# Kernel tuning notes

Measured on AMD Instinct MI355X. Metric: run time of the kernel, lower is better.

The kernel has to match this reference:

```python
import math
import itertools
import jax, jax.numpy as jnp
import numpy as np

SEQ_LEN = 16
D_IN = 2048
TSS = 3          # temporal_set_size
D_OUT = 1128
PE_SCALE = 0.1
N_SUPPORT = 5
N_QUERIES = 1
LN_EPS = 1e-5


def _pos_enc(seq_len, d_model):
    pos = np.arange(seq_len, dtype=np.float32)[:, None]
    div = np.exp(np.arange(0, d_model, 2, dtype=np.float32) * -(math.log(10000.0) / d_model))
    pe = np.zeros((seq_len, d_model), dtype=np.float32)
    pe[:, 0::2] = np.sin(pos * div) * PE_SCALE
    pe[:, 1::2] = np.cos(pos * div) * PE_SCALE
    return jnp.asarray(pe)


def _tuples(seq_len, k):
    return np.asarray(list(itertools.combinations(range(seq_len), k)), dtype=np.int32)  # [T, k]


def setup_inputs() -> dict:
    key = jax.random.key(0)
    ks = jax.random.split(key, 8)
    return {
        "support_set": jax.random.normal(ks[0], (N_SUPPORT, SEQ_LEN, D_IN), jnp.float32),
        "queries": jax.random.normal(ks[1], (N_QUERIES, SEQ_LEN, D_IN), jnp.float32),
        "support_labels": jnp.arange(N_SUPPORT, dtype=jnp.int64),
        "wk": jax.random.normal(ks[2], (D_OUT, D_IN * TSS), jnp.float32) * 0.02,
        "bk": jax.random.normal(ks[3], (D_OUT,), jnp.float32) * 0.02,
        "wv": jax.random.normal(ks[4], (D_OUT, D_IN * TSS), jnp.float32) * 0.02,
        "bv": jax.random.normal(ks[5], (D_OUT,), jnp.float32) * 0.02,
        "gamma": jnp.ones((D_OUT,), jnp.float32),
        "beta": jnp.zeros((D_OUT,), jnp.float32),
    }


def _layer_norm(x, gamma, beta):
    mu = jnp.mean(x, axis=-1, keepdims=True)
    var = jnp.mean(jnp.square(x - mu), axis=-1, keepdims=True)
    return (x - mu) * jax.lax.rsqrt(var + LN_EPS) * gamma + beta


def reference(support_set, queries, support_labels, wk, bk, wv, bv, gamma, beta):
    tup = _tuples(SEQ_LEN, TSS)                      # [T, 3] static
    T = tup.shape[0]                                 # tuples_len = C(16,3) = 560
    pe = _pos_enc(SEQ_LEN, D_IN)                     # [S, D_IN]

    s = support_set + pe                             # [5, S, D_IN]
    q = queries + pe                                 # [1, S, D_IN]

    # gather frame tuples and flatten: [n, T, 3*D_IN]
    s_t = s[:, tup, :].reshape(N_SUPPORT, T, TSS * D_IN)
    q_t = q[:, tup, :].reshape(N_QUERIES, T, TSS * D_IN)

    s_ks = _layer_norm(s_t @ wk.T + bk, gamma, beta)  # [5, T, D_OUT]
    q_ks = _layer_norm(q_t @ wk.T + bk, gamma, beta)  # [1, T, D_OUT]
    s_vs = s_t @ wv.T + bv                            # [5, T, D_OUT]
    q_vs = q_t @ wv.T + bv                            # [1, T, D_OUT]

    # _extract_class_indices returns the label value itself -> direct row gather
    ck = s_ks[support_labels]                         # [C, T, D_OUT]
    cv = s_vs[support_labels]                         # [C, T, D_OUT]

    scores = jnp.einsum('qtd,csd->cqts', q_ks, ck) / math.sqrt(D_OUT)  # [C, Q, T, T]
    attn = jax.nn.softmax(scores, axis=-1)            # softmax over support tuples
    proto = jnp.einsum('cqts,csd->cqtd', attn, cv)    # [C, Q, T, D_OUT]

    diff = q_vs[None] - proto                         # [C, Q, T, D_OUT]
    dist = -jnp.sum(diff * diff, axis=(-2, -1)) / T   # [C, Q]
    logits = dist.T                                   # [Q, C]
    return logits
```

## Files before the change

### kernel.cpp

```cpp
#include <hip/hip_runtime.h>
#include <hip/hip_bf16.h>

#define SEQ 16
#define DIN 2048
#define TSS 3
#define DOUT 1128
#define DPAD 1152
#define NT 560
#define NTPAD 576
#define NSEQ 6
#define NCOL 6768
#define W1CNT 6930432

typedef __attribute__((ext_vector_type(4))) float f32x4;
typedef __attribute__((ext_vector_type(8))) short bf16x8;

__device__ __forceinline__ float bf2f(unsigned short h) {
    union { unsigned int u; float f; } c; c.u = ((unsigned int)h) << 16; return c.f;
}
__device__ __forceinline__ unsigned short f2bf(float f) {
    union { float f; unsigned int u; } c; c.f = f;
    unsigned int lsb = (c.u >> 16) & 1;
    c.u += 0x7fffu + lsb;
    return (unsigned short)(c.u >> 16);
}
__device__ __forceinline__ float loadf(const void* p, size_t i, int f32m) {
    return f32m ? ((const float*)p)[i] : bf2f(((const unsigned short*)p)[i]);
}
__device__ __forceinline__ int probe_f32(const void* gamma) {
    return (((const unsigned int*)gamma)[0] == 0x3F800000u) ? 1 : 0;
}
__device__ __forceinline__ int probe_i64(const void* labels) {
    return (((const long long*)labels)[1] == 1LL) ? 1 : 0;
}
__device__ __forceinline__ int get_label(const void* p, int c, int is64) {
    long long v = is64 ? ((const long long*)p)[c] : (long long)((const int*)p)[c];
    if (v < 0) v = 0; if (v > 4) v = 4;
    return (int)v;
}


__global__ __launch_bounds__(256) void k_build_wx(
        const void* __restrict__ sup, const void* __restrict__ qry,
        const void* __restrict__ wk, const void* __restrict__ wv,
        const void* __restrict__ gamma,
        unsigned short* __restrict__ XF, unsigned short* __restrict__ WbF) {
    int f32m = probe_f32(gamma);
    if (blockIdx.x < 96) {
        int c8 = blockIdx.x * 256 + threadIdx.x;
        int idx512 = c8 >> 6;
        int rowgrp = idx512 >> 6, kt = idx512 & 63;
        int sub = c8 & 63;
        int r15 = sub & 15;
        int row = rowgrp * 16 + r15;
        int f = row & 15, n = row >> 4;
        int k = kt * 32 + (sub >> 4) * 8;
        bf16x8 ov;
#pragma unroll
        for (int j = 0; j < 8; ++j) {
            int d = k + j;
            float v = (n < 5) ? loadf(sup, (size_t)row * DIN + d, f32m)
                              : loadf(qry, (size_t)f * DIN + d, f32m);
            int m2 = d & ~1;
            float div = __expf(-(float)m2 * (9.210340371976184f / 2048.0f));
            float ang = (float)f * div;
            float pe = ((d & 1) ? __cosf(ang) : __sinf(ang)) * 0.1f;
            ov[j] = (short)f2bf(v + pe);
        }
        *(bf16x8*)(XF + (size_t)c8 * 8) = ov;
    } else {
        size_t c8 = (size_t)(blockIdx.x - 96) * 256 + threadIdx.x;
        size_t idx512 = c8 >> 6;
        int colgrp = (int)(idx512 >> 6);
        int kt = (int)(idx512 & 63);
        int sub = (int)(c8 & 63);
        int col = colgrp * 16 + (sub & 15);
        int k = kt * 32 + (sub >> 4) * 8;
        int which = col / 3384; int rem = col - which * 3384;
        int seg = rem / DOUT;   int o = rem - seg * DOUT;
        const void* src = which ? wv : wk;
        size_t si = (size_t)o * (TSS * DIN) + (size_t)seg * DIN + k;
        if (f32m) {
            f32x4 w0 = *(const f32x4*)((const float*)src + si);
            f32x4 w1 = *(const f32x4*)((const float*)src + si + 4);
            bf16x8 ov;
#pragma unroll
            for (int j = 0; j < 4; ++j) {
                ov[j]     = (short)f2bf(w0[j]);
                ov[4 + j] = (short)f2bf(w1[j]);
            }
            *(bf16x8*)(WbF + c8 * 8) = ov;
        } else {
            *(bf16x8*)(WbF + c8 * 8) = *(const bf16x8*)((const unsigned short*)src + si);
        }
    }
}

__global__ __launch_bounds__(256) void k_proj(
        const unsigned short* __restrict__ XF, const unsigned short* __restrict__ WbF,
        unsigned short* __restrict__ Pb) {
    int tn = blockIdx.x;
    int tid = threadIdx.x;
    int w = tid >> 6, lane = tid & 63;
    int c16 = lane & 15, quad = lane >> 4;
    int cg0 = tn * 2;
    int cg1 = (tn * 2 + 1 > 422) ? 422 : tn * 2 + 1;
    const unsigned short* bF0 = WbF + ((size_t)cg0 << 15) + lane * 8;
    const unsigned short* bF1 = WbF + ((size_t)cg1 << 15) + lane * 8;
    const unsigned short* aF  = XF + lane * 8;

    f32x4 acc[6][2];
#pragma unroll
    for (int m = 0; m < 6; ++m)
#pragma unroll
        for (int ch = 0; ch < 2; ++ch) acc[m][ch] = (f32x4){0.f, 0.f, 0.f, 0.f};

    int ktb = w * 16;
#pragma unroll 2
    for (int kt = ktb; kt < ktb + 16; ++kt) {
        bf16x8 b0 = *(const bf16x8*)(bF0 + ((size_t)kt << 9));
        bf16x8 b1 = *(const bf16x8*)(bF1 + ((size_t)kt << 9));
#pragma unroll
        for (int m = 0; m < 6; ++m) {
            bf16x8 a = *(const bf16x8*)(aF + ((size_t)(m * 64 + kt) << 9));
            acc[m][0] = __builtin_amdgcn_mfma_f32_16x16x32_bf16(a, b0, acc[m][0], 0, 0, 0);
            acc[m][1] = __builtin_amdgcn_mfma_f32_16x16x32_bf16(a, b1, acc[m][1], 0, 0, 0);
        }
    }
    __shared__ float red[3 * 12 * 64 * 4];
    if (w > 0) {
#pragma unroll
        for (int m = 0; m < 6; ++m)
#pragma unroll
            for (int ch = 0; ch < 2; ++ch)
#pragma unroll
                for (int r = 0; r < 4; ++r)
                    red[(((w - 1) * 12 + m * 2 + ch) * 64 + lane) * 4 + r] = acc[m][ch][r];
    }
    __syncthreads();
    if (w == 0) {
#pragma unroll
        for (int m = 0; m < 6; ++m)
#pragma unroll
            for (int ch = 0; ch < 2; ++ch) {
                int t = m * 2 + ch;
#pragma unroll
                for (int r = 0; r < 4; ++r) {
                    float s = acc[m][ch][r]
                            + red[((0 * 12 + t) * 64 + lane) * 4 + r]
                            + red[((1 * 12 + t) * 64 + lane) * 4 + r]
                            + red[((2 * 12 + t) * 64 + lane) * 4 + r];
                    int row = m * 16 + quad * 4 + r;
                    int col = tn * 32 + ch * 16 + c16;
                    if (col < NCOL) Pb[(size_t)row * NCOL + col] = f2bf(s);
                }
            }
    }
}

__global__ __launch_bounds__(256) void k_combine_ln(
        const unsigned short* __restrict__ Pb,
        const void* __restrict__ bk, const void* __restrict__ bv,
        const void* __restrict__ gamma, const void* __restrict__ beta,
        unsigned short* __restrict__ ksF, unsigned short* __restrict__ vs) {
    int n = blockIdx.x / NT, t = blockIdx.x % NT;
    int f32m = probe_f32(gamma);
    int idx = t, fi, fj, fk;
    for (fi = 0;; ++fi) { int c2 = (15 - fi) * (14 - fi) / 2; if (idx < c2) break; idx -= c2; }
    for (fj = fi + 1;; ++fj) { int c1 = 15 - fj; if (idx < c1) break; idx -= c1; }
    fk = fj + 1 + idx;
    size_t ri = (size_t)(n * 16 + fi) * NCOL;
    size_t rj = (size_t)(n * 16 + fj) * NCOL;
    size_t rk = (size_t)(n * 16 + fk) * NCOL;

    float kv[5], vv[5];
    float s = 0.f, s2 = 0.f;
#pragma unroll
    for (int it = 0; it < 5; ++it) {
        int o = threadIdx.x + it * 256;
        kv[it] = 0.f; vv[it] = 0.f;
        if (o < DOUT) {
            float a = bf2f(Pb[ri + o]) + bf2f(Pb[rj + DOUT + o])
                    + bf2f(Pb[rk + 2 * DOUT + o]) + loadf(bk, o, f32m);
            float b = bf2f(Pb[ri + 3 * DOUT + o]) + bf2f(Pb[rj + 4 * DOUT + o])
                    + bf2f(Pb[rk + 5 * DOUT + o]) + loadf(bv, o, f32m);
            kv[it] = a; vv[it] = b;
            s += a; s2 += a * a;
        }
    }
    __shared__ float red[8];
#pragma unroll
    for (int off = 32; off; off >>= 1) { s += __shfl_down(s, off); s2 += __shfl_down(s2, off); }
    int wid = threadIdx.x >> 6;
    if ((threadIdx.x & 63) == 0) { red[wid] = s; red[4 + wid] = s2; }
    __syncthreads();
    s = red[0] + red[1] + red[2] + red[3];
    s2 = red[4] + red[5] + red[6] + red[7];
    float mu = s / (float)DOUT;
    float var = s2 / (float)DOUT - mu * mu;
    float rstd = rsqrtf(var + 1e-5f);

    size_t ntbase = ((size_t)(n * 36 + (t >> 4)) * 36) * 512 + (size_t)(t & 15) * 8;
    size_t vbase = ((size_t)n * NT + t) * DPAD;
#pragma unroll
    for (int it = 0; it < 5; ++it) {
        int o = threadIdx.x + it * 256;
        if (o < DPAD) {
            float kres = 0.f;
            if (o < DOUT)
                kres = (kv[it] - mu) * rstd * loadf(gamma, o, f32m) + loadf(beta, o, f32m);
            ksF[ntbase + ((size_t)(o >> 5) << 9) + (((o >> 3) & 3) << 7) + (o & 7)] =
                (o < DOUT) ? f2bf(kres) : 0;
            vs[vbase + o] = (o < DOUT) ? f2bf(vv[it]) : 0;
        }
    }
}

__global__ __launch_bounds__(256) void k_transpose(
        const unsigned short* __restrict__ vs, unsigned short* __restrict__ vsTF) {
    int b = blockIdx.x;
    int tt = b % 18; b /= 18; int ot = b % 36; int n = b / 36;
    int t0 = tt * 32, o0 = ot * 32;
    int tx = threadIdx.x & 31, ty = threadIdx.x >> 5;
    __shared__ unsigned short tile[32][33];
#pragma unroll
    for (int i = 0; i < 4; ++i) {
        int t = t0 + ty + 8 * i;
        tile[ty + 8 * i][tx] = (t < NT) ? vs[((size_t)n * NT + t) * DPAD + o0 + tx] : 0;
    }
    __syncthreads();
#pragma unroll
    for (int i = 0; i < 4; ++i) {
        int r = ty + 8 * i;
        size_t addr = ((size_t)(n * 72 + ot * 2 + (r >> 4)) * 18 + tt) * 512
                    + (size_t)((tx >> 3) * 16 + (r & 15)) * 8 + (tx & 7);
        vsTF[addr] = tile[tx][r];
    }
}

__global__ __launch_bounds__(256) void k_scores(
        const unsigned short* __restrict__ ksF, const void* __restrict__ labels,
        float* __restrict__ scores) {
    int b = blockIdx.x;
    int c = b % 5; int rest = b / 5;
    int tm = rest / 9, tn = rest % 9;
    int tid = threadIdx.x;
    int w = tid >> 6, lane = tid & 63;
    int c16 = lane & 15, quad = lane >> 4;
    int lab = get_label(labels, c, probe_i64(labels));
    const unsigned short* aF[4];
    const unsigned short* bF[4];
#pragma unroll
    for (int i = 0; i < 4; ++i) {
        aF[i] = ksF + (((size_t)(5 * 36 + tm * 4 + i) * 36) << 9) + lane * 8;
        bF[i] = ksF + (((size_t)(lab * 36 + tn * 4 + i) * 36) << 9) + lane * 8;
    }
    f32x4 acc[4][4];
#pragma unroll
    for (int i = 0; i < 4; ++i)
#pragma unroll
        for (int j = 0; j < 4; ++j) acc[i][j] = (f32x4){0.f, 0.f, 0.f, 0.f};

    int ktb = w * 9;
#pragma unroll 2
    for (int kt = ktb; kt < ktb + 9; ++kt) {
        bf16x8 a[4], bv4[4];
#pragma unroll
        for (int i = 0; i < 4; ++i) a[i]   = *(const bf16x8*)(aF[i] + ((size_t)kt << 9));
#pragma unroll
        for (int j = 0; j < 4; ++j) bv4[j] = *(const bf16x8*)(bF[j] + ((size_t)kt << 9));
#pragma unroll
        for (int i = 0; i < 4; ++i)
#pragma unroll
            for (int j = 0; j < 4; ++j)
                acc[i][j] = __builtin_amdgcn_mfma_f32_16x16x32_bf16(a[i], bv4[j], acc[i][j], 0, 0, 0);
    }
    __shared__ float red[3 * 16 * 64 * 4];
    if (w > 0) {
#pragma unroll
        for (int i = 0; i < 4; ++i)
#pragma unroll
            for (int j = 0; j < 4; ++j)
#pragma unroll
                for (int r = 0; r < 4; ++r)
                    red[(((w - 1) * 16 + i * 4 + j) * 64 + lane) * 4 + r] = acc[i][j][r];
    }
    __syncthreads();
    if (w == 0) {
        const float scale = 0.029774540f;
#pragma unroll
        for (int i = 0; i < 4; ++i)
#pragma unroll
            for (int j = 0; j < 4; ++j) {
                int t = i * 4 + j;
#pragma unroll
                for (int r = 0; r < 4; ++r) {
                    float s = acc[i][j][r]
                            + red[((0 * 16 + t) * 64 + lane) * 4 + r]
                            + red[((1 * 16 + t) * 64 + lane) * 4 + r]
                            + red[((2 * 16 + t) * 64 + lane) * 4 + r];
                    int tq = tm * 64 + i * 16 + quad * 4 + r;
                    int ts = tn * 64 + j * 16 + c16;
                    scores[((size_t)c * NTPAD + tq) * NTPAD + ts] = s * scale;
                }
            }
    }
}

__global__ __launch_bounds__(256) void k_softmax(
        const float* __restrict__ scores, unsigned short* __restrict__ attnF) {
    int row = blockIdx.x * 4 + (threadIdx.x >> 6);
    int lane = threadIdx.x & 63;
    int c = row / NTPAD, tq = row % NTPAD;
    unsigned short* dstc = attnF + ((size_t)(c * 36 + (tq >> 4)) * 18) * 512 + (size_t)(tq & 15) * 8;
    if (tq >= NT) {
#pragma unroll
        for (int i = 0; i < 9; ++i) {
            int ts = lane + i * 64;
            dstc[((ts >> 5) << 9) + ((ts >> 3) & 3) * 128 + (ts & 7)] = 0;
        }
        return;
    }
    const float* src = scores + (size_t)row * NTPAD;
    float vals[9];
    float m = -1e30f;
#pragma unroll
    for (int i = 0; i < 9; ++i) {
        int idx = lane + i * 64;
        vals[i] = (idx < NT) ? src[idx] : -1e30f;
        m = fmaxf(m, vals[i]);
    }
#pragma unroll
    for (int off = 32; off; off >>= 1) m = fmaxf(m, __shfl_xor(m, off));
    float s = 0.f;
#pragma unroll
    for (int i = 0; i < 9; ++i) {
        int idx = lane + i * 64;
        vals[i] = (idx < NT) ? __expf(vals[i] - m) : 0.f;
        s += vals[i];
    }
#pragma unroll
    for (int off = 32; off; off >>= 1) s += __shfl_xor(s, off);
    float inv = 1.f / s;
#pragma unroll
    for (int i = 0; i < 9; ++i) {
        int ts = lane + i * 64;
        dstc[((ts >> 5) << 9) + ((ts >> 3) & 3) * 128 + (ts & 7)] =
            (ts < NT) ? f2bf(vals[i] * inv) : 0;
    }
}

__global__ __launch_bounds__(128) void k_proto_dist(
        const unsigned short* __restrict__ attnF, const unsigned short* __restrict__ vs,
        const unsigned short* __restrict__ vsTF,
        const void* __restrict__ labels, float* __restrict__ parts) {
    int b = blockIdx.x;
    int c = b / 162; int rest = b % 162;
    int tm = rest / 18, tn = rest % 18;
    int tid = threadIdx.x;
    int w = tid >> 6, lane = tid & 63;
    int c16 = lane & 15, quad = lane >> 4;
    int lab = get_label(labels, c, probe_i64(labels));
    const unsigned short* aF = attnF + ((size_t)(c * 36 + tm * 4) * 18) * 512 + lane * 8;
    const unsigned short* bF = vsTF + ((size_t)(lab * 72 + tn * 4) * 18) * 512 + lane * 8;
    f32x4 acc[4][4];
#pragma unroll
    for (int i = 0; i < 4; ++i)
#pragma unroll
        for (int j = 0; j < 4; ++j) acc[i][j] = (f32x4){0.f, 0.f, 0.f, 0.f};

    int ktb = w * 9;
#pragma unroll 2
    for (int kt = ktb; kt < ktb + 9; ++kt) {
        bf16x8 a[4], bv4[4];
#pragma unroll
        for (int i = 0; i < 4; ++i) a[i]   = *(const bf16x8*)(aF + ((size_t)(i * 18 + kt) << 9));
#pragma unroll
        for (int j = 0; j < 4; ++j) bv4[j] = *(const bf16x8*)(bF + ((size_t)(j * 18 + kt) << 9));
#pragma unroll
        for (int i = 0; i < 4; ++i)
#pragma unroll
            for (int j = 0; j < 4; ++j)
                acc[i][j] = __builtin_amdgcn_mfma_f32_16x16x32_bf16(a[i], bv4[j], acc[i][j], 0, 0, 0);
    }
    __shared__ float red[16 * 64 * 4];
    if (w == 1) {
#pragma unroll
        for (int i = 0; i < 4; ++i)
#pragma unroll
            for (int j = 0; j < 4; ++j)
#pragma unroll
                for (int r = 0; r < 4; ++r)
                    red[((i * 4 + j) * 64 + lane) * 4 + r] = acc[i][j][r];
    }
    __syncthreads();
    if (w == 0) {
        const unsigned short* qv = vs + (size_t)5 * NT * DPAD;
        float part = 0.f;
#pragma unroll
        for (int i = 0; i < 4; ++i)
#pragma unroll
            for (int j = 0; j < 4; ++j) {
                int t = i * 4 + j;
#pragma unroll
                for (int r = 0; r < 4; ++r) {
                    float s = acc[i][j][r] + red[(t * 64 + lane) * 4 + r];
                    int tq = tm * 64 + i * 16 + quad * 4 + r;
                    int o  = tn * 64 + j * 16 + c16;
                    if (tq < NT && o < DOUT) {
                        float d = bf2f(qv[(size_t)tq * DPAD + o]) - s;
                        part += d * d;
                    }
                }
            }
#pragma unroll
        for (int off = 32; off; off >>= 1) part += __shfl_down(part, off);
        if (lane == 0) parts[blockIdx.x] = part;
    }
}

__global__ __launch_bounds__(320) void k_final(const float* __restrict__ parts,
                                               const void* __restrict__ gamma,
                                               void* __restrict__ out) {
    int c = threadIdx.x >> 6;
    int lane = threadIdx.x & 63;
    float s = 0.f;
    for (int i = lane; i < 162; i += 64) s += parts[c * 162 + i];
#pragma unroll
    for (int off = 32; off; off >>= 1) s += __shfl_down(s, off);
    if (lane == 0) {
        float v = -s * (1.0f / (float)NT);
        if (probe_f32(gamma)) ((float*)out)[c] = v;
        else ((unsigned short*)out)[c] = f2bf(v);
    }
}

extern "C" void kernel_launch(void* const* d_in, const int* in_sizes, int n_in,
                              void* d_out, int out_size, void* d_ws, size_t ws_size,
                              hipStream_t stream) {
    const void* sup   = d_in[0];
    const void* qry   = d_in[1];
    const void* labs  = d_in[2];
    const void* wk    = d_in[3];
    const void* bk    = d_in[4];
    const void* wv    = d_in[5];
    const void* bv    = d_in[6];
    const void* gamma = d_in[7];
    const void* beta  = d_in[8];

    char* ws = (char*)d_ws;
    unsigned short* XF     = (unsigned short*)(ws + 256);
    unsigned short* Pb     = (unsigned short*)(ws + 393472);
    float*          parts  = (float*)(ws + 2992384);
    unsigned short* WbF    = (unsigned short*)(ws + 5604352);
    unsigned short* ksF    = (unsigned short*)(ws + 33326080);
    unsigned short* vsb    = (unsigned short*)(ws + 41288704);
    float*          scores = (float*)(ws + 49030144);
    unsigned short* attnF  = (unsigned short*)(ws + 55665664);
    unsigned short* vsTF   = (unsigned short*)(ws + 58983424);

    k_build_wx  <<<96 + 6768, 256, 0, stream>>>(sup, qry, wk, wv, gamma, XF, WbF);
    k_proj      <<<212, 256, 0, stream>>>(XF, WbF, Pb);
    k_combine_ln<<<NSEQ * NT, 256, 0, stream>>>(Pb, bk, bv, gamma, beta, ksF, vsb);
    k_transpose <<<5 * 36 * 18, 256, 0, stream>>>(vsb, vsTF);
    k_scores    <<<405, 256, 0, stream>>>(ksF, labs, scores);
    k_softmax   <<<720, 256, 0, stream>>>(scores, attnF);
    k_proto_dist<<<810, 128, 0, stream>>>(attnF, vsb, vsTF, labs, parts);
    k_final     <<<1, 320, 0, stream>>>(parts, gamma, d_out);
}
```

Before: 190.8 us.

## Fuse weight bf16 conversion into projection GEMM and merge transpose with scores

The separate pass that converted both fp32 weight matrices (about 55 MB read, 28 MB written) into a bf16 fragment layout is removed. The projection kernel now reads fp32 weights directly with strided per-lane loads and converts them to bf16 in registers before the MFMAs. This drops a large write and re-read of the converted weights, at the cost of less coalesced weight loads and conversion work inside the GEMM loop. Separately, the V transpose kernel is merged into the scores kernel as extra blocks so the two independent tasks share one launch.

```diff
diff --git a/kernel.cpp b/kernel.cpp
--- a/kernel.cpp
+++ b/kernel.cpp
@@ -10,7 +10,6 @@
 #define NTPAD 576
 #define NSEQ 6
 #define NCOL 6768
-#define W1CNT 6930432
 
 typedef __attribute__((ext_vector_type(4))) float f32x4;
 typedef __attribute__((ext_vector_type(8))) short bf16x8;
@@ -40,74 +39,52 @@
 }
 
 
-__global__ __launch_bounds__(256) void k_build_wx(
+__global__ __launch_bounds__(256) void k_build_x(
         const void* __restrict__ sup, const void* __restrict__ qry,
+        const void* __restrict__ gamma, unsigned short* __restrict__ XF) {
+    int f32m = probe_f32(gamma);
+    int c8 = blockIdx.x * 256 + threadIdx.x;
+    int idx512 = c8 >> 6;
+    int rowgrp = idx512 >> 6, kt = idx512 & 63;
+    int sub = c8 & 63;
+    int r15 = sub & 15;
+    int row = rowgrp * 16 + r15;
+    int f = row & 15, n = row >> 4;
+    int k = kt * 32 + (sub >> 4) * 8;
+    bf16x8 ov;
+#pragma unroll
+    for (int j = 0; j < 8; ++j) {
+        int d = k + j;
+        float v = (n < 5) ? loadf(sup, (size_t)row * DIN + d, f32m)
+                          : loadf(qry, (size_t)f * DIN + d, f32m);
+        int m2 = d & ~1;
+        float div = __expf(-(float)m2 * (9.210340371976184f / 2048.0f));
+        float ang = (float)f * div;
+        float pe = ((d & 1) ? __cosf(ang) : __sinf(ang)) * 0.1f;
+        ov[j] = (short)f2bf(v + pe);
+    }
+    *(bf16x8*)(XF + (size_t)c8 * 8) = ov;
+}
+
+__global__ __launch_bounds__(256) void k_proj(
+        const unsigned short* __restrict__ XF,
         const void* __restrict__ wk, const void* __restrict__ wv,
-        const void* __restrict__ gamma,
-        unsigned short* __restrict__ XF, unsigned short* __restrict__ WbF) {
-    int f32m = probe_f32(gamma);
-    if (blockIdx.x < 96) {
-        int c8 = blockIdx.x * 256 + threadIdx.x;
-        int idx512 = c8 >> 6;
-        int rowgrp = idx512 >> 6, kt = idx512 & 63;
-        int sub = c8 & 63;
-        int r15 = sub & 15;
-        int row = rowgrp * 16 + r15;
-        int f = row & 15, n = row >> 4;
-        int k = kt * 32 + (sub >> 4) * 8;
-        bf16x8 ov;
-#pragma unroll
-        for (int j = 0; j < 8; ++j) {
-            int d = k + j;
-            float v = (n < 5) ? loadf(sup, (size_t)row * DIN + d, f32m)
-                              : loadf(qry, (size_t)f * DIN + d, f32m);
-            int m2 = d & ~1;
-            float div = __expf(-(float)m2 * (9.210340371976184f / 2048.0f));
-            float ang = (float)f * div;
-            float pe = ((d & 1) ? __cosf(ang) : __sinf(ang)) * 0.1f;
-            ov[j] = (short)f2bf(v + pe);
-        }
-        *(bf16x8*)(XF + (size_t)c8 * 8) = ov;
-    } else {
-        size_t c8 = (size_t)(blockIdx.x - 96) * 256 + threadIdx.x;
-        size_t idx512 = c8 >> 6;
-        int colgrp = (int)(idx512 >> 6);
-        int kt = (int)(idx512 & 63);
-        int sub = (int)(c8 & 63);
-        int col = colgrp * 16 + (sub & 15);
-        int k = kt * 32 + (sub >> 4) * 8;
-        int which = col / 3384; int rem = col - which * 3384;
-        int seg = rem / DOUT;   int o = rem - seg * DOUT;
-        const void* src = which ? wv : wk;
-        size_t si = (size_t)o * (TSS * DIN) + (size_t)seg * DIN + k;
-        if (f32m) {
-            f32x4 w0 = *(const f32x4*)((const float*)src + si);
-            f32x4 w1 = *(const f32x4*)((const float*)src + si + 4);
-            bf16x8 ov;
-#pragma unroll
-            for (int j = 0; j < 4; ++j) {
-                ov[j]     = (short)f2bf(w0[j]);
-                ov[4 + j] = (short)f2bf(w1[j]);
-            }
-            *(bf16x8*)(WbF + c8 * 8) = ov;
-        } else {
-            *(bf16x8*)(WbF + c8 * 8) = *(const bf16x8*)((const unsigned short*)src + si);
-        }
-    }
-}
-
-__global__ __launch_bounds__(256) void k_proj(
-        const unsigned short* __restrict__ XF, const unsigned short* __restrict__ WbF,
-        unsigned short* __restrict__ Pb) {
+        const void* __restrict__ gamma, unsigned short* __restrict__ Pb) {
     int tn = blockIdx.x;
     int tid = threadIdx.x;
     int w = tid >> 6, lane = tid & 63;
     int c16 = lane & 15, quad = lane >> 4;
-    int cg0 = tn * 2;
-    int cg1 = (tn * 2 + 1 > 422) ? 422 : tn * 2 + 1;
-    const unsigned short* bF0 = WbF + ((size_t)cg0 << 15) + lane * 8;
-    const unsigned short* bF1 = WbF + ((size_t)cg1 << 15) + lane * 8;
-    const unsigned short* aF  = XF + lane * 8;
+    int colA = tn * 32 + c16;
+    int colB0 = colA + 16;
+    int colB = colB0 > 6767 ? 6767 : colB0;
+    int whA = colA / 3384; int reA = colA - whA * 3384;
+    int sgA = reA / DOUT;  int oA  = reA - sgA * DOUT;
+    int whB = colB / 3384; int reB = colB - whB * 3384;
+    int sgB = reB / DOUT;  int oB  = reB - sgB * DOUT;
+    size_t offA = (size_t)oA * (TSS * DIN) + (size_t)sgA * DIN;
+    size_t offB = (size_t)oB * (TSS * DIN) + (size_t)sgB * DIN;
+    int f32m = probe_f32(gamma);
+    const unsigned short* aF = XF + lane * 8;
 
     f32x4 acc[6][2];
 #pragma unroll
@@ -115,16 +92,44 @@
 #pragma unroll
         for (int ch = 0; ch < 2; ++ch) acc[m][ch] = (f32x4){0.f, 0.f, 0.f, 0.f};
 
-    int ktb = w * 16;
+    int kb = w * 512;
+    if (f32m) {
+        const float* wA = (const float*)(whA ? wv : wk) + offA;
+        const float* wB = (const float*)(whB ? wv : wk) + offB;
 #pragma unroll 2
-    for (int kt = ktb; kt < ktb + 16; ++kt) {
-        bf16x8 b0 = *(const bf16x8*)(bF0 + ((size_t)kt << 9));
-        bf16x8 b1 = *(const bf16x8*)(bF1 + ((size_t)kt << 9));
-#pragma unroll
-        for (int m = 0; m < 6; ++m) {
-            bf16x8 a = *(const bf16x8*)(aF + ((size_t)(m * 64 + kt) << 9));
-            acc[m][0] = __builtin_amdgcn_mfma_f32_16x16x32_bf16(a, b0, acc[m][0], 0, 0, 0);
-            acc[m][1] = __builtin_amdgcn_mfma_f32_16x16x32_bf16(a, b1, acc[m][1], 0, 0, 0);
+        for (int k0 = kb; k0 < kb + 512; k0 += 32) {
+            f32x4 a0 = *(const f32x4*)(wA + k0 + quad * 8);
+            f32x4 a1 = *(const f32x4*)(wA + k0 + quad * 8 + 4);
+            f32x4 c0 = *(const f32x4*)(wB + k0 + quad * 8);
+            f32x4 c1 = *(const f32x4*)(wB + k0 + quad * 8 + 4);
+            bf16x8 b0, b1;
+#pragma unroll
+            for (int j = 0; j < 4; ++j) {
+                b0[j] = (short)f2bf(a0[j]); b0[4 + j] = (short)f2bf(a1[j]);
+                b1[j] = (short)f2bf(c0[j]); b1[4 + j] = (short)f2bf(c1[j]);
+            }
+            int kt = k0 >> 5;
+#pragma unroll
+            for (int m = 0; m < 6; ++m) {
+                bf16x8 a = *(const bf16x8*)(aF + ((size_t)(m * 64 + kt) << 9));
+                acc[m][0] = __builtin_amdgcn_mfma_f32_16x16x32_bf16(a, b0, acc[m][0], 0, 0, 0);
+                acc[m][1] = __builtin_amdgcn_mfma_f32_16x16x32_bf16(a, b1, acc[m][1], 0, 0, 0);
+            }
+        }
+    } else {
+        const unsigned short* wA = (const unsigned short*)(whA ? wv : wk) + offA;
+        const unsigned short* wB = (const unsigned short*)(whB ? wv : wk) + offB;
+#pragma unroll 2
+        for (int k0 = kb; k0 < kb + 512; k0 += 32) {
+            bf16x8 b0 = *(const bf16x8*)(wA + k0 + quad * 8);
+            bf16x8 b1 = *(const bf16x8*)(wB + k0 + quad * 8);
+            int kt = k0 >> 5;
+#pragma unroll
+            for (int m = 0; m < 6; ++m) {
+                bf16x8 a = *(const bf16x8*)(aF + ((size_t)(m * 64 + kt) << 9));
+                acc[m][0] = __builtin_amdgcn_mfma_f32_16x16x32_bf16(a, b0, acc[m][0], 0, 0, 0);
+                acc[m][1] = __builtin_amdgcn_mfma_f32_16x16x32_bf16(a, b1, acc[m][1], 0, 0, 0);
+            }
         }
     }
     __shared__ float red[3 * 12 * 64 * 4];
@@ -216,94 +221,95 @@
     }
 }
 
-__global__ __launch_bounds__(256) void k_transpose(
-        const unsigned short* __restrict__ vs, unsigned short* __restrict__ vsTF) {
-    int b = blockIdx.x;
-    int tt = b % 18; b /= 18; int ot = b % 36; int n = b / 36;
-    int t0 = tt * 32, o0 = ot * 32;
-    int tx = threadIdx.x & 31, ty = threadIdx.x >> 5;
-    __shared__ unsigned short tile[32][33];
-#pragma unroll
-    for (int i = 0; i < 4; ++i) {
-        int t = t0 + ty + 8 * i;
-        tile[ty + 8 * i][tx] = (t < NT) ? vs[((size_t)n * NT + t) * DPAD + o0 + tx] : 0;
-    }
-    __syncthreads();
-#pragma unroll
-    for (int i = 0; i < 4; ++i) {
-        int r = ty + 8 * i;
-        size_t addr = ((size_t)(n * 72 + ot * 2 + (r >> 4)) * 18 + tt) * 512
-                    + (size_t)((tx >> 3) * 16 + (r & 15)) * 8 + (tx & 7);
-        vsTF[addr] = tile[tx][r];
-    }
-}
-
-__global__ __launch_bounds__(256) void k_scores(
-        const unsigned short* __restrict__ ksF, const void* __restrict__ labels,
-        float* __restrict__ scores) {
-    int b = blockIdx.x;
-    int c = b % 5; int rest = b / 5;
-    int tm = rest / 9, tn = rest % 9;
-    int tid = threadIdx.x;
-    int w = tid >> 6, lane = tid & 63;
-    int c16 = lane & 15, quad = lane >> 4;
-    int lab = get_label(labels, c, probe_i64(labels));
-    const unsigned short* aF[4];
-    const unsigned short* bF[4];
-#pragma unroll
-    for (int i = 0; i < 4; ++i) {
-        aF[i] = ksF + (((size_t)(5 * 36 + tm * 4 + i) * 36) << 9) + lane * 8;
-        bF[i] = ksF + (((size_t)(lab * 36 + tn * 4 + i) * 36) << 9) + lane * 8;
-    }
-    f32x4 acc[4][4];
-#pragma unroll
-    for (int i = 0; i < 4; ++i)
-#pragma unroll
-        for (int j = 0; j < 4; ++j) acc[i][j] = (f32x4){0.f, 0.f, 0.f, 0.f};
-
-    int ktb = w * 9;
+__global__ __launch_bounds__(256) void k_scores_trans(
+        const unsigned short* __restrict__ ksF, const unsigned short* __restrict__ vs,
+        const void* __restrict__ labels,
+        float* __restrict__ scores, unsigned short* __restrict__ vsTF) {
+    __shared__ __align__(16) char smem[49152];
+    if (blockIdx.x < 405) {
+        float* red = (float*)smem;
+        int b = blockIdx.x;
+        int c = b % 5; int rest = b / 5;
+        int tm = rest / 9, tn = rest % 9;
+        int tid = threadIdx.x;
+        int w = tid >> 6, lane = tid & 63;
+        int c16 = lane & 15, quad = lane >> 4;
+        int lab = get_label(labels, c, probe_i64(labels));
+        const unsigned short* aF[4];
+        const unsigned short* bF[4];
+#pragma unroll
+        for (int i = 0; i < 4; ++i) {
+            aF[i] = ksF + (((size_t)(5 * 36 + tm * 4 + i) * 36) << 9) + lane * 8;
+            bF[i] = ksF + (((size_t)(lab * 36 + tn * 4 + i) * 36) << 9) + lane * 8;
+        }
+        f32x4 acc[4][4];
+#pragma unroll
+        for (int i = 0; i < 4; ++i)
+#pragma unroll
+            for (int j = 0; j < 4; ++j) acc[i][j] = (f32x4){0.f, 0.f, 0.f, 0.f};
+        int ktb = w * 9;
 #pragma unroll 2
-    for (int kt = ktb; kt < ktb + 9; ++kt) {
-        bf16x8 a[4], bv4[4];
-#pragma unroll
-        for (int i = 0; i < 4; ++i) a[i]   = *(const bf16x8*)(aF[i] + ((size_t)kt << 9));
-#pragma unroll
-        for (int j = 0; j < 4; ++j) bv4[j] = *(const bf16x8*)(bF[j] + ((size_t)kt << 9));
-#pragma unroll
-        for (int i = 0; i < 4; ++i)
-#pragma unroll
-            for (int j = 0; j < 4; ++j)
-                acc[i][j] = __builtin_amdgcn_mfma_f32_16x16x32_bf16(a[i], bv4[j], acc[i][j], 0, 0, 0);
-    }
-    __shared__ float red[3 * 16 * 64 * 4];
-    if (w > 0) {
-#pragma unroll
-        for (int i = 0; i < 4; ++i)
-#pragma unroll
-            for (int j = 0; j < 4; ++j)
-#pragma unroll
-                for (int r = 0; r < 4; ++r)
-                    red[(((w - 1) * 16 + i * 4 + j) * 64 + lane) * 4 + r] = acc[i][j][r];
-    }
-    __syncthreads();
-    if (w == 0) {
-        const float scale = 0.029774540f;
-#pragma unroll
-        for (int i = 0; i < 4; ++i)
-#pragma unroll
-            for (int j = 0; j < 4; ++j) {
-                int t = i * 4 + j;
-#pragma unroll
-                for (int r = 0; r < 4; ++r) {
-                    float s = acc[i][j][r]
-                            + red[((0 * 16 + t) * 64 + lane) * 4 + r]
-                            + red[((1 * 16 + t) * 64 + lane) * 4 + r]
-                            + red[((2 * 16 + t) * 64 + lane) * 4 + r];
-                    int tq = tm * 64 + i * 16 + quad * 4 + r;
-                    int ts = tn * 64 + j * 16 + c16;
-                    scores[((size_t)c * NTPAD + tq) * NTPAD + ts] = s * scale;
+        for (int kt = ktb; kt < ktb + 9; ++kt) {
+            bf16x8 a[4], bv4[4];
+#pragma unroll
+            for (int i = 0; i < 4; ++i) a[i]   = *(const bf16x8*)(aF[i] + ((size_t)kt << 9));
+#pragma unroll
+            for (int j = 0; j < 4; ++j) bv4[j] = *(const bf16x8*)(bF[j] + ((size_t)kt << 9));
+#pragma unroll
+            for (int i = 0; i < 4; ++i)
+#pragma unroll
+                for (int j = 0; j < 4; ++j)
+                    acc[i][j] = __builtin_amdgcn_mfma_f32_16x16x32_bf16(a[i], bv4[j], acc[i][j], 0, 0, 0);
+        }
+        if (w > 0) {
+#pragma unroll
+            for (int i = 0; i < 4; ++i)
+#pragma unroll
+                for (int j = 0; j < 4; ++j)
+#pragma unroll
+                    for (int r = 0; r < 4; ++r)
+                        red[(((w - 1) * 16 + i * 4 + j) * 64 + lane) * 4 + r] = acc[i][j][r];
+        }
+        __syncthreads();
+        if (w == 0) {
+            const float scale = 0.029774540f;
+#pragma unroll
+            for (int i = 0; i < 4; ++i)
+#pragma unroll
+                for (int j = 0; j < 4; ++j) {
+                    int t = i * 4 + j;
+#pragma unroll
+                    for (int r = 0; r < 4; ++r) {
+                        float s = acc[i][j][r]
+                                + red[((0 * 16 + t) * 64 + lane) * 4 + r]
+                                + red[((1 * 16 + t) * 64 + lane) * 4 + r]
+                                + red[((2 * 16 + t) * 64 + lane) * 4 + r];
+                        int tq = tm * 64 + i * 16 + quad * 4 + r;
+                        int ts = tn * 64 + j * 16 + c16;
+                        scores[((size_t)c * NTPAD + tq) * NTPAD + ts] = s * scale;
+                    }
                 }
-            }
+        }
+    } else {
+        typedef unsigned short tile_t[33];
+        tile_t* tile = (tile_t*)smem;
+        int b = blockIdx.x - 405;
+        int tt = b % 18; b /= 18; int ot = b % 36; int n = b / 36;
+        int t0 = tt * 32, o0 = ot * 32;
+        int tx = threadIdx.x & 31, ty = threadIdx.x >> 5;
+#pragma unroll
+        for (int i = 0; i < 4; ++i) {
+            int t = t0 + ty + 8 * i;
+            tile[ty + 8 * i][tx] = (t < NT) ? vs[((size_t)n * NT + t) * DPAD + o0 + tx] : 0;
+        }
+        __syncthreads();
+#pragma unroll
+        for (int i = 0; i < 4; ++i) {
+            int r = ty + 8 * i;
+            size_t addr = ((size_t)(n * 72 + ot * 2 + (r >> 4)) * 18 + tt) * 512
+                        + (size_t)((tx >> 3) * 16 + (r & 15)) * 8 + (tx & 7);
+            vsTF[addr] = tile[tx][r];
+        }
     }
 }
 
@@ -452,19 +458,17 @@
     unsigned short* XF     = (unsigned short*)(ws + 256);
     unsigned short* Pb     = (unsigned short*)(ws + 393472);
     float*          parts  = (float*)(ws + 2992384);
-    unsigned short* WbF    = (unsigned short*)(ws + 5604352);
     unsigned short* ksF    = (unsigned short*)(ws + 33326080);
     unsigned short* vsb    = (unsigned short*)(ws + 41288704);
     float*          scores = (float*)(ws + 49030144);
     unsigned short* attnF  = (unsigned short*)(ws + 55665664);
     unsigned short* vsTF   = (unsigned short*)(ws + 58983424);
 
-    k_build_wx  <<<96 + 6768, 256, 0, stream>>>(sup, qry, wk, wv, gamma, XF, WbF);
-    k_proj      <<<212, 256, 0, stream>>>(XF, WbF, Pb);
-    k_combine_ln<<<NSEQ * NT, 256, 0, stream>>>(Pb, bk, bv, gamma, beta, ksF, vsb);
-    k_transpose <<<5 * 36 * 18, 256, 0, stream>>>(vsb, vsTF);
-    k_scores    <<<405, 256, 0, stream>>>(ksF, labs, scores);
-    k_softmax   <<<720, 256, 0, stream>>>(scores, attnF);
-    k_proto_dist<<<810, 128, 0, stream>>>(attnF, vsb, vsTF, labs, parts);
-    k_final     <<<1, 320, 0, stream>>>(parts, gamma, d_out);
-}
+    k_build_x     <<<96, 256, 0, stream>>>(sup, qry, gamma, XF);
+    k_proj        <<<212, 256, 0, stream>>>(XF, wk, wv, gamma, Pb);
+    k_combine_ln  <<<NSEQ * NT, 256, 0, stream>>>(Pb, bk, bv, gamma, beta, ksF, vsb);
+    k_scores_trans<<<405 + 3240, 256, 0, stream>>>(ksF, vsb, labs, scores, vsTF);
+    k_softmax     <<<720, 256, 0, stream>>>(scores, attnF);
+    k_proto_dist  <<<810, 128, 0, stream>>>(attnF, vsb, vsTF, labs, parts);
+    k_final       <<<1, 320, 0, stream>>>(parts, gamma, d_out);
+}
```

Result: slower. 207.0 us (+8.5%).
